# Kernel tuning notes

Hardware: AMD Instinct MI355X
Metric: run time of the kernel (lower is better)

## Reference

```python
import jax, jax.numpy as jnp
import numpy as np

B, S, F, H = 64, 2048, 512, 512

def setup_inputs() -> dict:
    key = jax.random.key(0)
    ks = jax.random.split(key, 9)
    def xavier(k, shape):
        lim = float(np.sqrt(6.0 / (shape[0] + shape[1])))
        return jax.random.uniform(k, shape, jnp.float32, -lim, lim)
    inp = {"x": jax.random.normal(ks[0], (B, S, F), jnp.float32)}
    names = ["ii", "hi", "if_", "hf", "ig", "hg", "io", "ho"]
    for i, nm in enumerate(names):
        in_dim = F if nm[0] == "i" else H
        inp["w_" + nm] = xavier(ks[i + 1], (in_dim, H))
        inp["b_" + nm] = jnp.zeros((H,), jnp.float32)
    return inp

def reference(x, w_ii, b_ii, w_hi, b_hi, w_if_, b_if_, w_hf, b_hf,
              w_ig, b_ig, w_hg, b_hg, w_io, b_io, w_ho, b_ho):
    b = x.shape[0]
    h0 = jnp.zeros((b, w_hi.shape[0]), x.dtype)
    c0 = jnp.zeros_like(h0)
    # Precompute input projections for all timesteps (one big GEMM each):
    xi = jnp.einsum('bsf,fh->bsh', x, w_ii) + b_ii + b_hi  # fold both biases
    xf = jnp.einsum('bsf,fh->bsh', x, w_if_) + b_if_ + b_hf
    xg = jnp.einsum('bsf,fh->bsh', x, w_ig) + b_ig + b_hg
    xo = jnp.einsum('bsf,fh->bsh', x, w_io) + b_io + b_ho
    xs = jnp.stack([xi, xf, xg, xo], axis=0).transpose(2, 0, 1, 3)  # [S,4,B,H]

    def step(carry, x_t):
        h, c = carry
        i = jax.nn.sigmoid(x_t[0] + h @ w_hi)
        f = jax.nn.sigmoid(x_t[1] + h @ w_hf)
        g = jnp.tanh(x_t[2] + h @ w_hg)
        o = jax.nn.sigmoid(x_t[3] + h @ w_ho)
        c_new = f * c + i * g
        h_new = o * jnp.tanh(c_new)
        return (h_new, c_new), None

    (h_t, c_t), _ = jax.lax.scan(step, (h0, c0), xs)
    return (h_t, c_t)
```

## Files before the change

### kernel.cpp

```cpp
#include <hip/hip_runtime.h>

typedef unsigned short u16;
typedef unsigned int u32;
typedef unsigned long long u64;
typedef short short8 __attribute__((ext_vector_type(8)));
typedef float floatx4 __attribute__((ext_vector_type(4)));
typedef u32 u32x4 __attribute__((ext_vector_type(4)));

#define SLEN 2048
#define BATCH 64
#define FDIM 512
#define HDIM 512
#define NWG 128
#define NTH 320
#define GROUPS 4
#define ROWS 16
#define HROW_U32 (HDIM/2)
#define HGRP_U32 (ROWS*HROW_U32)
#define HB_U32 (GROUPS*HGRP_U32)
#define NRING 4
#define WS_BYTES (NRING*HB_U32*4)
#define SENT 0xFFFFFFFFu

#define LDS_W_U16 (4*16*64*8)
#define XR 20

__device__ __forceinline__ u16 f2bf_rne(float f) {
  union { float f; u32 u; } v; v.f = f;
  u32 u = v.u + 0x7FFFu + ((v.u >> 16) & 1u);
  return (u16)(u >> 16);
}
__device__ __forceinline__ float sigmoidf_fast(float x) {
  return 1.0f / (1.0f + __expf(-x));
}
__device__ __forceinline__ float tanhf_fast(float x) {
  return 1.0f - 2.0f / (__expf(2.0f * x) + 1.0f);
}

__device__ __forceinline__ void x_gemm1(
    const float* __restrict__ xrow, const u16* __restrict__ lds_wx,
    int gt, int lane, int n, int kq, float* __restrict__ sd)
{
  floatx4 a0 = {0.f, 0.f, 0.f, 0.f};
#pragma unroll
  for (int kk = 0; kk < 16; ++kk) {
    floatx4 xa = *(const floatx4*)(xrow + kk*32 + kq*8);
    floatx4 xb = *(const floatx4*)(xrow + kk*32 + kq*8 + 4);
    short8 ax;
#pragma unroll
    for (int j = 0; j < 4; ++j) {
      ax[j]     = (short)f2bf_rne(xa[j]);
      ax[4 + j] = (short)f2bf_rne(xb[j]);
    }
    short8 b0 = *(const short8*)&lds_wx[((gt*16 + kk)*64 + lane)*8];
    a0 = __builtin_amdgcn_mfma_f32_16x16x32_bf16(ax, b0, a0, 0, 0, 0);
  }
  *(floatx4*)(sd + ((size_t)gt*16 + n)*XR + kq*4) = a0;
}

#define HL(I, OFF) \
  asm volatile("global_load_dwordx4 %0, %1, off offset:" OFF " sc0 sc1" \
               : "=v"(hv[I]) : "v"(hp))

__global__ __launch_bounds__(NTH, 1)
void lstm_persistent(
    const float* __restrict__ x,
    const float* __restrict__ w_ii, const float* __restrict__ b_ii,
    const float* __restrict__ w_hi, const float* __restrict__ b_hi,
    const float* __restrict__ w_if, const float* __restrict__ b_if,
    const float* __restrict__ w_hf, const float* __restrict__ b_hf,
    const float* __restrict__ w_ig, const float* __restrict__ b_ig,
    const float* __restrict__ w_hg, const float* __restrict__ b_hg,
    const float* __restrict__ w_io, const float* __restrict__ b_io,
    const float* __restrict__ w_ho, const float* __restrict__ b_ho,
    float* __restrict__ out, u32* __restrict__ hbuf)
{
  __shared__ __align__(16) u16 lds_wh[LDS_W_U16];
  __shared__ __align__(16) u16 lds_wx[LDS_W_U16];
  __shared__ __align__(16) float scr_x[4][4][16][XR];

  const int tid  = threadIdx.x;
  const int g    = blockIdx.x & 3;
  const int c    = blockIdx.x >> 2;
  const int wv   = tid >> 6;
  const int lane = tid & 63;
  const int n    = lane & 15;
  const int kq   = lane >> 4;

  {
    const float* WH[4] = {w_hi, w_hf, w_hg, w_ho};
    const float* WX[4] = {w_ii, w_if, w_ig, w_io};
    for (int idx = tid; idx < 4*512*16; idx += NTH) {
      int col  = idx & 15;
      int k    = (idx >> 4) & 511;
      int gt   = idx >> 13;
      int kk   = k >> 5, rem = k & 31, quad = rem >> 3, j = rem & 7;
      int di   = ((gt*16 + kk)*64 + quad*16 + col)*8 + j;
      int src  = k*HDIM + c*16 + col;
      lds_wh[di] = f2bf_rne(WH[gt][src]);
      lds_wx[di] = f2bf_rne(WX[gt][src]);
    }
  }

  const int col = c*16 + n;
  const float bias0 = b_ii[col] + b_hi[col];
  const float bias1 = b_if[col] + b_hf[col];
  const float bias2 = b_ig[col] + b_hg[col];
  const float bias3 = b_io[col] + b_ho[col];
  floatx4 c_st = {0.f, 0.f, 0.f, 0.f};

  const float* xbase = x + (size_t)(g*ROWS + n) * (SLEN * FDIM);

  __syncthreads();

  if (wv >= 1) {
    x_gemm1(xbase,        lds_wx, wv - 1, lane, n, kq, &scr_x[0][0][0][0]);
    x_gemm1(xbase + FDIM, lds_wx, wv - 1, lane, n, kq, &scr_x[1][0][0][0]);
  }

  for (int t = 0; t < SLEN; ++t) {
    __syncthreads();

    if (wv >= 1) {
      if (t + 2 < SLEN)
        x_gemm1(xbase + (size_t)(t + 2)*FDIM, lds_wx, wv - 1, lane, n, kq,
                &scr_x[(t + 2) & 3][0][0][0]);
    } else {
      const float* sx = &scr_x[t & 3][0][0][0];
      floatx4 sxv0 = *(const floatx4*)(sx + (0*16 + n)*XR + kq*4);
      floatx4 sxv1 = *(const floatx4*)(sx + (1*16 + n)*XR + kq*4);
      floatx4 sxv2 = *(const floatx4*)(sx + (2*16 + n)*XR + kq*4);
      floatx4 sxv3 = *(const floatx4*)(sx + (3*16 + n)*XR + kq*4);

      floatx4 acc0 = {0.f,0.f,0.f,0.f}, acc1 = {0.f,0.f,0.f,0.f};
      floatx4 acc2 = {0.f,0.f,0.f,0.f}, acc3 = {0.f,0.f,0.f,0.f};

      if (t > 0) {
        const u32* hp = hbuf + (size_t)(t & 3)*HB_U32 + g*HGRP_U32 + n*HROW_U32 + kq*4;
        u32x4 hv[16];
        int ready;
        do {
          HL(0,"0");   HL(1,"64");  HL(2,"128"); HL(3,"192");
          HL(4,"256"); HL(5,"320"); HL(6,"384"); HL(7,"448");
          HL(8,"512"); HL(9,"576"); HL(10,"640"); HL(11,"704");
          HL(12,"768"); HL(13,"832"); HL(14,"896"); HL(15,"960");
          asm volatile("s_waitcnt vmcnt(0)" ::: "memory");
          __builtin_amdgcn_sched_barrier(0);
          u32 mx = 0u;
#pragma unroll
          for (int i = 0; i < 16; ++i) {
#pragma unroll
            for (int j = 0; j < 4; ++j) {
              u32 w = hv[i][j];
              mx = (w > mx) ? w : mx;
            }
          }
          ready = __all((int)(mx != SENT));
        } while (!ready);

        {
          u32* rz = hbuf + (size_t)((t - 1) & 3)*HB_U32 + g*HGRP_U32;
          int i0 = lane, i1 = lane + 64;
          __hip_atomic_store(&rz[(i0 >> 3)*HROW_U32 + c*8 + (i0 & 7)], SENT,
                             __ATOMIC_RELAXED, __HIP_MEMORY_SCOPE_AGENT);
          __hip_atomic_store(&rz[(i1 >> 3)*HROW_U32 + c*8 + (i1 & 7)], SENT,
                             __ATOMIC_RELAXED, __HIP_MEMORY_SCOPE_AGENT);
        }

#pragma unroll
        for (int kk = 0; kk < 16; ++kk) {
          union { u32x4 u; short8 s; } ha; ha.u = hv[kk];
          acc0 = __builtin_amdgcn_mfma_f32_16x16x32_bf16(ha.s, *(const short8*)&lds_wh[((0*16+kk)*64+lane)*8], acc0, 0,0,0);
          acc1 = __builtin_amdgcn_mfma_f32_16x16x32_bf16(ha.s, *(const short8*)&lds_wh[((1*16+kk)*64+lane)*8], acc1, 0,0,0);
          acc2 = __builtin_amdgcn_mfma_f32_16x16x32_bf16(ha.s, *(const short8*)&lds_wh[((2*16+kk)*64+lane)*8], acc2, 0,0,0);
          acc3 = __builtin_amdgcn_mfma_f32_16x16x32_bf16(ha.s, *(const short8*)&lds_wh[((3*16+kk)*64+lane)*8], acc3, 0,0,0);
        }
      }

      float hnew[4];
#pragma unroll
      for (int r = 0; r < 4; ++r) {
        float gi = sigmoidf_fast(acc0[r] + sxv0[r] + bias0);
        float gf = sigmoidf_fast(acc1[r] + sxv1[r] + bias1);
        float gg = tanhf_fast  (acc2[r] + sxv2[r] + bias2);
        float go = sigmoidf_fast(acc3[r] + sxv3[r] + bias3);
        c_st[r] = gf * c_st[r] + gi * gg;
        hnew[r] = go * tanhf_fast(c_st[r]);
      }

      if (t == SLEN - 1) {
#pragma unroll
        for (int r = 0; r < 4; ++r) {
          int row = g*ROWS + kq*4 + r;
          out[row*HDIM + col]              = hnew[r];
          out[BATCH*HDIM + row*HDIM + col] = c_st[r];
        }
      } else {
        u32 hb[4];
#pragma unroll
        for (int r = 0; r < 4; ++r) hb[r] = (u32)f2bf_rne(hnew[r]);
        u32* hdst = hbuf + (size_t)((t + 1) & 3)*HB_U32 + g*HGRP_U32;
#pragma unroll
        for (int r = 0; r < 4; ++r) {
          u32 o = (u32)__shfl_xor((int)hb[r], 1);
          if ((n & 1) == 0) {
            u32 val = (o << 16) | hb[r];
            __hip_atomic_store(&hdst[(kq*4 + r)*HROW_U32 + c*8 + (n >> 1)],
                               val, __ATOMIC_RELAXED, __HIP_MEMORY_SCOPE_AGENT);
          }
        }
      }
    }
  }
}

extern "C" void kernel_launch(void* const* d_in, const int* in_sizes, int n_in,
                              void* d_out, int out_size, void* d_ws, size_t ws_size,
                              hipStream_t stream) {
  u32* hbuf = (u32*)d_ws;
  (void)hipMemsetAsync(d_ws, 0xFF, WS_BYTES, stream);

  lstm_persistent<<<dim3(NWG), dim3(NTH), 0, stream>>>(
      (const float*)d_in[0],
      (const float*)d_in[1],  (const float*)d_in[2],
      (const float*)d_in[3],  (const float*)d_in[4],
      (const float*)d_in[5],  (const float*)d_in[6],
      (const float*)d_in[7],  (const float*)d_in[8],
      (const float*)d_in[9],  (const float*)d_in[10],
      (const float*)d_in[11], (const float*)d_in[12],
      (const float*)d_in[13], (const float*)d_in[14],
      (const float*)d_in[15], (const float*)d_in[16],
      (float*)d_out, hbuf);
}
```

Before: 9.909 ms.

## Split recurrent GEMM across four waves with register weights and LDS flag sync

The recurrent h@W GEMM now runs on four waves, each doing a K-slice with its weight fragments held in registers, where before one wave did all 64 MFMAs per step. The partial sums are reduced through LDS. The four x-projection waves run ahead on an 8-slot ring and hand off through per-wave LDS flags instead of block-wide __syncthreads. This is meant to shorten the serial critical path of each timestep and decouple the x producers from the h consumer. The cost is an extra LDS reduction, spin-wait flag traffic, and higher register pressure at 512 threads.

```diff
diff --git a/kernel.cpp b/kernel.cpp
--- a/kernel.cpp
+++ b/kernel.cpp
@@ -2,7 +2,6 @@
 
 typedef unsigned short u16;
 typedef unsigned int u32;
-typedef unsigned long long u64;
 typedef short short8 __attribute__((ext_vector_type(8)));
 typedef float floatx4 __attribute__((ext_vector_type(4)));
 typedef u32 u32x4 __attribute__((ext_vector_type(4)));
@@ -12,7 +11,7 @@
 #define FDIM 512
 #define HDIM 512
 #define NWG 128
-#define NTH 320
+#define NTH 512
 #define GROUPS 4
 #define ROWS 16
 #define HROW_U32 (HDIM/2)
@@ -22,8 +21,15 @@
 #define WS_BYTES (NRING*HB_U32*4)
 #define SENT 0xFFFFFFFFu
 
-#define LDS_W_U16 (4*16*64*8)
-#define XR 20
+#define XSLOTS 8
+#define TILE_F (16*20)
+#define SCRH_F (16*TILE_F)
+#define SCRX_SLOT_F (4*TILE_F)
+#define SCRX_F (XSLOTS*SCRX_SLOT_F)
+
+#define ARENA_BYTES 131072
+#define OFF_SCRX (SCRH_F*4)
+#define OFF_FLAGS (OFF_SCRX + SCRX_F*4)
 
 __device__ __forceinline__ u16 f2bf_rne(float f) {
   union { float f; u32 u; } v; v.f = f;
@@ -36,31 +42,6 @@
 __device__ __forceinline__ float tanhf_fast(float x) {
   return 1.0f - 2.0f / (__expf(2.0f * x) + 1.0f);
 }
-
-__device__ __forceinline__ void x_gemm1(
-    const float* __restrict__ xrow, const u16* __restrict__ lds_wx,
-    int gt, int lane, int n, int kq, float* __restrict__ sd)
-{
-  floatx4 a0 = {0.f, 0.f, 0.f, 0.f};
-#pragma unroll
-  for (int kk = 0; kk < 16; ++kk) {
-    floatx4 xa = *(const floatx4*)(xrow + kk*32 + kq*8);
-    floatx4 xb = *(const floatx4*)(xrow + kk*32 + kq*8 + 4);
-    short8 ax;
-#pragma unroll
-    for (int j = 0; j < 4; ++j) {
-      ax[j]     = (short)f2bf_rne(xa[j]);
-      ax[4 + j] = (short)f2bf_rne(xb[j]);
-    }
-    short8 b0 = *(const short8*)&lds_wx[((gt*16 + kk)*64 + lane)*8];
-    a0 = __builtin_amdgcn_mfma_f32_16x16x32_bf16(ax, b0, a0, 0, 0, 0);
-  }
-  *(floatx4*)(sd + ((size_t)gt*16 + n)*XR + kq*4) = a0;
-}
-
-#define HL(I, OFF) \
-  asm volatile("global_load_dwordx4 %0, %1, off offset:" OFF " sc0 sc1" \
-               : "=v"(hv[I]) : "v"(hp))
 
 __global__ __launch_bounds__(NTH, 1)
 void lstm_persistent(
@@ -75,9 +56,7 @@
     const float* __restrict__ w_ho, const float* __restrict__ b_ho,
     float* __restrict__ out, u32* __restrict__ hbuf)
 {
-  __shared__ __align__(16) u16 lds_wh[LDS_W_U16];
-  __shared__ __align__(16) u16 lds_wx[LDS_W_U16];
-  __shared__ __align__(16) float scr_x[4][4][16][XR];
+  __shared__ __align__(16) char arena[ARENA_BYTES];
 
   const int tid  = threadIdx.x;
   const int g    = blockIdx.x & 3;
@@ -87,129 +66,201 @@
   const int n    = lane & 15;
   const int kq   = lane >> 4;
 
+  u16* lds_wh = (u16*)arena;
+  u16* lds_wx = (u16*)(arena + 65536);
+
   {
     const float* WH[4] = {w_hi, w_hf, w_hg, w_ho};
     const float* WX[4] = {w_ii, w_if, w_ig, w_io};
     for (int idx = tid; idx < 4*512*16; idx += NTH) {
-      int col  = idx & 15;
-      int k    = (idx >> 4) & 511;
-      int gt   = idx >> 13;
-      int kk   = k >> 5, rem = k & 31, quad = rem >> 3, j = rem & 7;
-      int di   = ((gt*16 + kk)*64 + quad*16 + col)*8 + j;
-      int src  = k*HDIM + c*16 + col;
+      int col = idx & 15;
+      int k   = (idx >> 4) & 511;
+      int gt  = idx >> 13;
+      int kk  = k >> 5, rem = k & 31, quad = rem >> 3, j = rem & 7;
+      int di  = ((gt*16 + kk)*64 + quad*16 + col)*8 + j;
+      int src = k*HDIM + c*16 + col;
       lds_wh[di] = f2bf_rne(WH[gt][src]);
       lds_wx[di] = f2bf_rne(WX[gt][src]);
     }
   }
-
-  const int col = c*16 + n;
-  const float bias0 = b_ii[col] + b_hi[col];
-  const float bias1 = b_if[col] + b_hf[col];
-  const float bias2 = b_ig[col] + b_hg[col];
-  const float bias3 = b_io[col] + b_ho[col];
-  floatx4 c_st = {0.f, 0.f, 0.f, 0.f};
-
-  const float* xbase = x + (size_t)(g*ROWS + n) * (SLEN * FDIM);
-
   __syncthreads();
 
-  if (wv >= 1) {
-    x_gemm1(xbase,        lds_wx, wv - 1, lane, n, kq, &scr_x[0][0][0][0]);
-    x_gemm1(xbase + FDIM, lds_wx, wv - 1, lane, n, kq, &scr_x[1][0][0][0]);
+  short8 wf[16];
+  if (wv < 4) {
+#pragma unroll
+    for (int gt = 0; gt < 4; ++gt)
+#pragma unroll
+      for (int kkl = 0; kkl < 4; ++kkl)
+        wf[gt*4 + kkl] = *(const short8*)&lds_wh[((gt*16 + wv*4 + kkl)*64 + lane)*8];
+  } else {
+    const int gt = wv - 4;
+#pragma unroll
+    for (int kk = 0; kk < 16; ++kk)
+      wf[kk] = *(const short8*)&lds_wx[((gt*16 + kk)*64 + lane)*8];
   }
-
-  for (int t = 0; t < SLEN; ++t) {
-    __syncthreads();
-
-    if (wv >= 1) {
-      if (t + 2 < SLEN)
-        x_gemm1(xbase + (size_t)(t + 2)*FDIM, lds_wx, wv - 1, lane, n, kq,
-                &scr_x[(t + 2) & 3][0][0][0]);
-    } else {
-      const float* sx = &scr_x[t & 3][0][0][0];
-      floatx4 sxv0 = *(const floatx4*)(sx + (0*16 + n)*XR + kq*4);
-      floatx4 sxv1 = *(const floatx4*)(sx + (1*16 + n)*XR + kq*4);
-      floatx4 sxv2 = *(const floatx4*)(sx + (2*16 + n)*XR + kq*4);
-      floatx4 sxv3 = *(const floatx4*)(sx + (3*16 + n)*XR + kq*4);
-
-      floatx4 acc0 = {0.f,0.f,0.f,0.f}, acc1 = {0.f,0.f,0.f,0.f};
-      floatx4 acc2 = {0.f,0.f,0.f,0.f}, acc3 = {0.f,0.f,0.f,0.f};
+  __syncthreads();
+
+  float* scr_h = (float*)arena;
+  float* scr_x = (float*)(arena + OFF_SCRX);
+  int*   flg   = (int*)(arena + OFF_FLAGS);
+  if (tid < 16) flg[tid] = -1;
+  __syncthreads();
+
+  if (wv < 4) {
+    const int w     = wv;
+    const int row_e = w*4 + kq;
+    const int colg  = c*16 + n;
+    const float b0 = b_ii[colg] + b_hi[colg];
+    const float b1 = b_if[colg] + b_hf[colg];
+    const float b2 = b_ig[colg] + b_hg[colg];
+    const float b3 = b_io[colg] + b_ho[colg];
+    float c_st = 0.f;
+
+    for (int t = 0; t < SLEN; ++t) {
+      floatx4 a0 = {0.f,0.f,0.f,0.f}, a1 = {0.f,0.f,0.f,0.f};
+      floatx4 a2 = {0.f,0.f,0.f,0.f}, a3 = {0.f,0.f,0.f,0.f};
 
       if (t > 0) {
-        const u32* hp = hbuf + (size_t)(t & 3)*HB_U32 + g*HGRP_U32 + n*HROW_U32 + kq*4;
-        u32x4 hv[16];
+        const u32* hp = hbuf + (size_t)(t & 3)*HB_U32 + g*HGRP_U32
+                      + n*HROW_U32 + w*64 + kq*4;
+        u32x4 hv0, hv1, hv2, hv3;
         int ready;
         do {
-          HL(0,"0");   HL(1,"64");  HL(2,"128"); HL(3,"192");
-          HL(4,"256"); HL(5,"320"); HL(6,"384"); HL(7,"448");
-          HL(8,"512"); HL(9,"576"); HL(10,"640"); HL(11,"704");
-          HL(12,"768"); HL(13,"832"); HL(14,"896"); HL(15,"960");
+          asm volatile("global_load_dwordx4 %0, %1, off sc0 sc1"            : "=v"(hv0) : "v"(hp));
+          asm volatile("global_load_dwordx4 %0, %1, off offset:64 sc0 sc1"  : "=v"(hv1) : "v"(hp));
+          asm volatile("global_load_dwordx4 %0, %1, off offset:128 sc0 sc1" : "=v"(hv2) : "v"(hp));
+          asm volatile("global_load_dwordx4 %0, %1, off offset:192 sc0 sc1" : "=v"(hv3) : "v"(hp));
           asm volatile("s_waitcnt vmcnt(0)" ::: "memory");
           __builtin_amdgcn_sched_barrier(0);
           u32 mx = 0u;
 #pragma unroll
-          for (int i = 0; i < 16; ++i) {
-#pragma unroll
-            for (int j = 0; j < 4; ++j) {
-              u32 w = hv[i][j];
-              mx = (w > mx) ? w : mx;
-            }
+          for (int j = 0; j < 4; ++j) {
+            mx = hv0[j] > mx ? hv0[j] : mx;
+            mx = hv1[j] > mx ? hv1[j] : mx;
+            mx = hv2[j] > mx ? hv2[j] : mx;
+            mx = hv3[j] > mx ? hv3[j] : mx;
           }
           ready = __all((int)(mx != SENT));
         } while (!ready);
 
-        {
-          u32* rz = hbuf + (size_t)((t - 1) & 3)*HB_U32 + g*HGRP_U32;
-          int i0 = lane, i1 = lane + 64;
-          __hip_atomic_store(&rz[(i0 >> 3)*HROW_U32 + c*8 + (i0 & 7)], SENT,
-                             __ATOMIC_RELAXED, __HIP_MEMORY_SCOPE_AGENT);
-          __hip_atomic_store(&rz[(i1 >> 3)*HROW_U32 + c*8 + (i1 & 7)], SENT,
-                             __ATOMIC_RELAXED, __HIP_MEMORY_SCOPE_AGENT);
+        union { u32x4 u; short8 s; } h0, h1, h2, h3;
+        h0.u = hv0; h1.u = hv1; h2.u = hv2; h3.u = hv3;
+        a0 = __builtin_amdgcn_mfma_f32_16x16x32_bf16(h0.s, wf[0],  a0, 0,0,0);
+        a1 = __builtin_amdgcn_mfma_f32_16x16x32_bf16(h0.s, wf[4],  a1, 0,0,0);
+        a2 = __builtin_amdgcn_mfma_f32_16x16x32_bf16(h0.s, wf[8],  a2, 0,0,0);
+        a3 = __builtin_amdgcn_mfma_f32_16x16x32_bf16(h0.s, wf[12], a3, 0,0,0);
+        a0 = __builtin_amdgcn_mfma_f32_16x16x32_bf16(h1.s, wf[1],  a0, 0,0,0);
+        a1 = __builtin_amdgcn_mfma_f32_16x16x32_bf16(h1.s, wf[5],  a1, 0,0,0);
+        a2 = __builtin_amdgcn_mfma_f32_16x16x32_bf16(h1.s, wf[9],  a2, 0,0,0);
+        a3 = __builtin_amdgcn_mfma_f32_16x16x32_bf16(h1.s, wf[13], a3, 0,0,0);
+        a0 = __builtin_amdgcn_mfma_f32_16x16x32_bf16(h2.s, wf[2],  a0, 0,0,0);
+        a1 = __builtin_amdgcn_mfma_f32_16x16x32_bf16(h2.s, wf[6],  a1, 0,0,0);
+        a2 = __builtin_amdgcn_mfma_f32_16x16x32_bf16(h2.s, wf[10], a2, 0,0,0);
+        a3 = __builtin_amdgcn_mfma_f32_16x16x32_bf16(h2.s, wf[14], a3, 0,0,0);
+        a0 = __builtin_amdgcn_mfma_f32_16x16x32_bf16(h3.s, wf[3],  a0, 0,0,0);
+        a1 = __builtin_amdgcn_mfma_f32_16x16x32_bf16(h3.s, wf[7],  a1, 0,0,0);
+        a2 = __builtin_amdgcn_mfma_f32_16x16x32_bf16(h3.s, wf[11], a2, 0,0,0);
+        a3 = __builtin_amdgcn_mfma_f32_16x16x32_bf16(h3.s, wf[15], a3, 0,0,0);
+      }
+
+#pragma unroll
+      for (int i = 0; i < 4; ++i)
+        while (__hip_atomic_load(&flg[12+i], __ATOMIC_RELAXED, __HIP_MEMORY_SCOPE_WORKGROUP) < t-1) {}
+      asm volatile("" ::: "memory");
+
+      *(floatx4*)&scr_h[((w*4 + 0)*16 + n)*20 + kq*4] = a0;
+      *(floatx4*)&scr_h[((w*4 + 1)*16 + n)*20 + kq*4] = a1;
+      *(floatx4*)&scr_h[((w*4 + 2)*16 + n)*20 + kq*4] = a2;
+      *(floatx4*)&scr_h[((w*4 + 3)*16 + n)*20 + kq*4] = a3;
+      asm volatile("s_waitcnt lgkmcnt(0)" ::: "memory");
+      __hip_atomic_store(&flg[w], t, __ATOMIC_RELAXED, __HIP_MEMORY_SCOPE_WORKGROUP);
+
+#pragma unroll
+      for (int i = 0; i < 4; ++i)
+        while (__hip_atomic_load(&flg[i], __ATOMIC_RELAXED, __HIP_MEMORY_SCOPE_WORKGROUP) < t) {}
+#pragma unroll
+      for (int i = 0; i < 4; ++i)
+        while (__hip_atomic_load(&flg[4+i], __ATOMIC_RELAXED, __HIP_MEMORY_SCOPE_WORKGROUP) < t) {}
+      asm volatile("" ::: "memory");
+
+      if (t > 0 && lane < 32) {
+        int rr = w*4 + (lane >> 3);
+        int wd = lane & 7;
+        __hip_atomic_store(&hbuf[(size_t)((t-1) & 3)*HB_U32 + g*HGRP_U32
+                                 + rr*HROW_U32 + c*8 + wd],
+                           SENT, __ATOMIC_RELAXED, __HIP_MEMORY_SCOPE_AGENT);
+      }
+
+      float s0 = 0.f, s1 = 0.f, s2 = 0.f, s3 = 0.f;
+#pragma unroll
+      for (int w2 = 0; w2 < 4; ++w2) {
+        s0 += scr_h[((w2*4 + 0)*16 + n)*20 + row_e];
+        s1 += scr_h[((w2*4 + 1)*16 + n)*20 + row_e];
+        s2 += scr_h[((w2*4 + 2)*16 + n)*20 + row_e];
+        s3 += scr_h[((w2*4 + 3)*16 + n)*20 + row_e];
+      }
+      const float* sxp = scr_x + (size_t)(t & 7)*SCRX_SLOT_F;
+      float x0 = sxp[(0*16 + n)*20 + row_e];
+      float x1 = sxp[(1*16 + n)*20 + row_e];
+      float x2 = sxp[(2*16 + n)*20 + row_e];
+      float x3 = sxp[(3*16 + n)*20 + row_e];
+
+      float gi = sigmoidf_fast(s0 + x0 + b0);
+      float gf = sigmoidf_fast(s1 + x1 + b1);
+      float gg = tanhf_fast  (s2 + x2 + b2);
+      float go = sigmoidf_fast(s3 + x3 + b3);
+      c_st = gf * c_st + gi * gg;
+      float h_new = go * tanhf_fast(c_st);
+
+      if (t == SLEN - 1) {
+        int row = g*ROWS + row_e;
+        out[row*HDIM + colg]              = h_new;
+        out[BATCH*HDIM + row*HDIM + colg] = c_st;
+      } else {
+        u32 hb = (u32)f2bf_rne(h_new);
+        u32 o  = (u32)__shfl_xor((int)hb, 1);
+        asm volatile("s_waitcnt vmcnt(0)" ::: "memory");
+        if ((n & 1) == 0) {
+          u32 val = (o << 16) | hb;
+          __hip_atomic_store(&hbuf[(size_t)((t+1) & 3)*HB_U32 + g*HGRP_U32
+                                   + row_e*HROW_U32 + c*8 + (n >> 1)],
+                             val, __ATOMIC_RELAXED, __HIP_MEMORY_SCOPE_AGENT);
         }
-
-#pragma unroll
-        for (int kk = 0; kk < 16; ++kk) {
-          union { u32x4 u; short8 s; } ha; ha.u = hv[kk];
-          acc0 = __builtin_amdgcn_mfma_f32_16x16x32_bf16(ha.s, *(const short8*)&lds_wh[((0*16+kk)*64+lane)*8], acc0, 0,0,0);
-          acc1 = __builtin_amdgcn_mfma_f32_16x16x32_bf16(ha.s, *(const short8*)&lds_wh[((1*16+kk)*64+lane)*8], acc1, 0,0,0);
-          acc2 = __builtin_amdgcn_mfma_f32_16x16x32_bf16(ha.s, *(const short8*)&lds_wh[((2*16+kk)*64+lane)*8], acc2, 0,0,0);
-          acc3 = __builtin_amdgcn_mfma_f32_16x16x32_bf16(ha.s, *(const short8*)&lds_wh[((3*16+kk)*64+lane)*8], acc3, 0,0,0);
+      }
+
+      asm volatile("" ::: "memory");
+      __hip_atomic_store(&flg[8+w],  t, __ATOMIC_RELAXED, __HIP_MEMORY_SCOPE_WORKGROUP);
+      __hip_atomic_store(&flg[12+w], t, __ATOMIC_RELAXED, __HIP_MEMORY_SCOPE_WORKGROUP);
+    }
+  } else {
+    const int gt = wv - 4;
+    const float* xbase = x + (size_t)(g*ROWS + n) * (SLEN * FDIM);
+
+    for (int u = 0; u < SLEN; ++u) {
+      if (u >= XSLOTS) {
+        const int lim = u - XSLOTS;
+#pragma unroll
+        for (int i = 0; i < 4; ++i)
+          while (__hip_atomic_load(&flg[8+i], __ATOMIC_RELAXED, __HIP_MEMORY_SCOPE_WORKGROUP) < lim) {}
+        asm volatile("" ::: "memory");
+      }
+      const float* xrow = xbase + (size_t)u * FDIM;
+      floatx4 acc = {0.f,0.f,0.f,0.f};
+#pragma unroll
+      for (int kk = 0; kk < 16; ++kk) {
+        floatx4 xa = *(const floatx4*)(xrow + kk*32 + kq*8);
+        floatx4 xb = *(const floatx4*)(xrow + kk*32 + kq*8 + 4);
+        short8 ax;
+#pragma unroll
+        for (int j = 0; j < 4; ++j) {
+          ax[j]     = (short)f2bf_rne(xa[j]);
+          ax[4 + j] = (short)f2bf_rne(xb[j]);
         }
-      }
-
-      float hnew[4];
-#pragma unroll
-      for (int r = 0; r < 4; ++r) {
-        float gi = sigmoidf_fast(acc0[r] + sxv0[r] + bias0);
-        float gf = sigmoidf_fast(acc1[r] + sxv1[r] + bias1);
-        float gg = tanhf_fast  (acc2[r] + sxv2[r] + bias2);
-        float go = sigmoidf_fast(acc3[r] + sxv3[r] + bias3);
-        c_st[r] = gf * c_st[r] + gi * gg;
-        hnew[r] = go * tanhf_fast(c_st[r]);
-      }
-
-      if (t == SLEN - 1) {
-#pragma unroll
-        for (int r = 0; r < 4; ++r) {
-          int row = g*ROWS + kq*4 + r;
-          out[row*HDIM + col]              = hnew[r];
-          out[BATCH*HDIM + row*HDIM + col] = c_st[r];
-        }
-      } else {
-        u32 hb[4];
-#pragma unroll
-        for (int r = 0; r < 4; ++r) hb[r] = (u32)f2bf_rne(hnew[r]);
-        u32* hdst = hbuf + (size_t)((t + 1) & 3)*HB_U32 + g*HGRP_U32;
-#pragma unroll
-        for (int r = 0; r < 4; ++r) {
-          u32 o = (u32)__shfl_xor((int)hb[r], 1);
-          if ((n & 1) == 0) {
-            u32 val = (o << 16) | hb[r];
-            __hip_atomic_store(&hdst[(kq*4 + r)*HROW_U32 + c*8 + (n >> 1)],
-                               val, __ATOMIC_RELAXED, __HIP_MEMORY_SCOPE_AGENT);
-          }
-        }
-      }
+        acc = __builtin_amdgcn_mfma_f32_16x16x32_bf16(ax, wf[kk], acc, 0, 0, 0);
+      }
+      *(floatx4*)&scr_x[(size_t)(u & 7)*SCRX_SLOT_F + (gt*16 + n)*20 + kq*4] = acc;
+      asm volatile("s_waitcnt lgkmcnt(0)" ::: "memory");
+      __hip_atomic_store(&flg[4+gt], u, __ATOMIC_RELAXED, __HIP_MEMORY_SCOPE_WORKGROUP);
     }
   }
 }
@@ -217,6 +268,7 @@
 extern "C" void kernel_launch(void* const* d_in, const int* in_sizes, int n_in,
                               void* d_out, int out_size, void* d_ws, size_t ws_size,
                               hipStream_t stream) {
+  (void)in_sizes; (void)n_in; (void)out_size; (void)ws_size;
   u32* hbuf = (u32*)d_ws;
   (void)hipMemsetAsync(d_ws, 0xFF, WS_BYTES, stream);
 
```

Result: slower. 12.30 ms (+24.1%).
